# Performance work log

Hardware: AMD Instinct MI355X
Metric: run time of the kernel (lower is better)

## Reference

```python
import jax, jax.numpy as jnp
import numpy as np

B, N, D = 4, 2048, 256
EPS = 1e-5


def _clinear(Z, W, b):
    # complex linear: Z (B,2,N,din), W (2,dout,din), b (2,dout)
    Zr, Zi = Z[:, 0], Z[:, 1]
    Wr, Wi = W[0], W[1]
    outr = Zr @ Wr.T - Zi @ Wi.T + b[0]
    outi = Zr @ Wi.T + Zi @ Wr.T + b[1]
    return jnp.stack([outr, outi], axis=1)


def setup_inputs() -> dict:
    key = jax.random.key(0)
    ks = jax.random.split(key, 14)
    sc = 1.0 / np.sqrt(D).astype(np.float32)
    t = jnp.tile(jnp.arange(N + 1, dtype=jnp.float32)[None] * 0.01, (B, 1))
    return {
        'Z_q': jax.random.normal(ks[0], (B, 2, N, D), jnp.float32),
        'Z_k': jax.random.normal(ks[1], (B, 2, N, D), jnp.float32),
        'Z_v': jax.random.normal(ks[2], (B, 2, N, D), jnp.float32),
        't_measure_all': t,
        'W_q': jax.random.normal(ks[3], (2, D, D), jnp.float32) * sc,
        'b_q': jax.random.normal(ks[4], (2, D), jnp.float32) * 0.01,
        'W_k': jax.random.normal(ks[5], (2, D, D), jnp.float32) * sc,
        'b_k': jax.random.normal(ks[6], (2, D), jnp.float32) * 0.01,
        'W_v': jax.random.normal(ks[7], (2, D, D), jnp.float32) * sc,
        'b_v': jax.random.normal(ks[8], (2, D), jnp.float32) * 0.01,
        'W_p': jax.random.normal(ks[9], (2, D, D), jnp.float32) * sc,
        'b_p': jax.random.normal(ks[10], (2, D), jnp.float32) * 0.01,
        'lambda1': jax.random.normal(ks[11], (2, D // 2, 1), jnp.float32),
        'lambda_Omega_sqrt': jax.random.normal(ks[12], (1, D, 1), jnp.float32) * sc,
        'lambda_Gamma_sqrt': jax.random.normal(ks[13], (1, D, 1), jnp.float32) * sc,
        'tau': jnp.asarray(1.0, jnp.float32),
        'delta': jnp.asarray(0.0, jnp.float32),
        'lambda_C': jnp.ones((1, D, 1), jnp.float32),
    }


def reference(Z_q, Z_k, Z_v, t_measure_all, W_q, b_q, W_k, b_k, W_v, b_v,
              W_p, b_p, lambda1, lambda_Omega_sqrt, lambda_Gamma_sqrt,
              tau, delta, lambda_C):
    # lambda_h = 0 * compute_lambda_h(lambda1): conjugate-pair spectrum, zeroed in forward
    lam_r = 0.0 * jnp.concatenate([lambda1[0], lambda1[0]], axis=0)[:, 0]   # (D,)
    lam_i = 0.0 * jnp.concatenate([lambda1[1], -lambda1[1]], axis=0)[:, 0]  # (D,)
    lam_Om = lambda_Omega_sqrt ** 2 + EPS   # process noise (1,D,1)
    lam_Ga = lambda_Gamma_sqrt ** 2 + EPS   # measurement noise (1,D,1)

    Q = _clinear(Z_q, W_q, b_q)  # (B,2,N,D)
    K = _clinear(Z_k, W_k, b_k)
    V = _clinear(Z_v, W_v, b_v)

    t = t_measure_all[0, :-1]  # (N,)
    # exponential state-transition kernels exp(+/- lambda * t): (2,N,D)
    mag_f = jnp.exp(lam_r[None] * t[:, None]); ph_f = lam_i[None] * t[:, None]
    exp_f = jnp.stack([mag_f * jnp.cos(ph_f), mag_f * jnp.sin(ph_f)])
    mag_b = jnp.exp(-lam_r[None] * t[:, None]); ph_b = -lam_i[None] * t[:, None]
    exp_b = jnp.stack([mag_b * jnp.cos(ph_b), mag_b * jnp.sin(ph_b)])
    # one-step transition exp(lambda * dt): (2,D)
    dt = t[1] - t[0]
    mat_exp = jnp.stack([jnp.exp(lam_r * dt) * jnp.cos(lam_i * dt),
                         jnp.exp(lam_r * dt) * jnp.sin(lam_i * dt)])

    # averaged covariance kernel, exact lambda->0 limit: Gamma + Omega*|t_i-t_j|, mean over D
    lamC2 = lambda_C[0, :, 0] ** 2
    ga_bar = jnp.mean(lamC2 * lam_Ga[0, :, 0])
    om_bar = jnp.mean(lamC2 * lam_Om[0, :, 0])
    abs_dt = jnp.abs(t[:, None] - t[None, :])          # (N,N)
    V_avg_ij = ga_bar + om_bar * abs_dt                # (N,N)

    # factorized kernels
    V_v = exp_f[None]                 # (1,2,N,D)
    U_q = exp_b[None] * Q             # (B,2,N,D)
    U_k = exp_b[None] * K
    U_v = exp_b[None] * V

    # precision-weighted squared residual norm R_ij = sum_d |V_k|^2 |U_q_i - U_k_j|^2
    Vk_abs = jnp.sum(exp_f ** 2, axis=0)              # (N,D)
    Uk_abs = jnp.sum(U_k ** 2, axis=1)                # (B,N,D)
    Uq_abs = jnp.sum(U_q ** 2, axis=1)                # (B,N,D)
    T1 = jnp.einsum('id,bjd->bij', Vk_abs, Uk_abs)
    T2 = jnp.sum(Vk_abs[None] * Uq_abs, axis=2)[:, :, None]
    T3 = (jnp.einsum('bid,bjd->bij', Vk_abs[None] * U_q[:, 0], U_k[:, 0]) +
          jnp.einsum('bid,bjd->bij', Vk_abs[None] * U_q[:, 1], U_k[:, 1]))
    R_qk_abs = T1 + T2 - 2.0 * T3                     # (B,N,N)

    scores = -(tau ** 2) * jnp.log(V_avg_ij[None] + R_qk_abs)
    mask = jnp.tril(jnp.ones((N, N), bool))
    scores = jnp.where(mask[None], scores, -jnp.inf)
    A = jax.nn.softmax(scores, axis=2)                # (B,N,N)
    Q_ij = jnp.stack([A, jnp.zeros_like(A)], axis=1)  # (B,2,N,N)

    # est_inner = complex matmul(Q_ij, U_v); Q imag part is zero
    est_inner = jnp.stack([jnp.einsum('bij,bjd->bid', A, U_v[:, 0]),
                           jnp.einsum('bij,bjd->bid', A, U_v[:, 1])], axis=1)
    est_v = V_v * est_inner          # plain elementwise product, as in source
    s = jax.nn.sigmoid(delta)
    est_eigenbasis = (1.0 - s) * V + s * est_v        # (B,2,N,D)

    # complex Hadamard with one-step transition
    pr = mat_exp[0][None, None] * est_eigenbasis[:, 0] - mat_exp[1][None, None] * est_eigenbasis[:, 1]
    pi = mat_exp[0][None, None] * est_eigenbasis[:, 1] + mat_exp[1][None, None] * est_eigenbasis[:, 0]
    pred_p = jnp.stack([pr, pi], axis=1)
    out = _clinear(pred_p, W_p, b_p)                  # (B,2,N,D)

    lambda_h = jnp.stack([lam_r, lam_i])[..., None]
    return est_eigenbasis, out, Q_ij, V_v, U_v, lambda_h
```

## Files before the change

kernel.cpp:

```cpp
#include <hip/hip_runtime.h>
#include <math.h>

#define BN 4
#define NN 2048
#define DD 256
#define EPSF 1e-5f

typedef __attribute__((ext_vector_type(8))) short bf16x8;
typedef __attribute__((ext_vector_type(4))) float f32x4;

constexpr size_t OFF_EST = 0;
constexpr size_t OFF_OUT = (size_t)BN * 2 * NN * DD;
constexpr size_t OFF_QIJ = OFF_OUT + (size_t)BN * 2 * NN * DD;
constexpr size_t OFF_VV  = OFF_QIJ + (size_t)BN * 2 * NN * NN;
constexpr size_t OFF_UV  = OFF_VV + (size_t)2 * NN * DD;
constexpr size_t OFF_LH  = OFF_UV + (size_t)BN * 2 * NN * DD;

constexpr size_t SCR_B0   = OFF_QIJ + (size_t)NN * NN;
constexpr size_t U_Q16    = 0;
constexpr size_t U_K16    = (size_t)BN * NN * DD;
constexpr size_t U_VT16   = 2 * (size_t)BN * NN * DD;
constexpr size_t SCR_QN   = SCR_B0 + 3 * (size_t)BN * NN * DD / 2;
constexpr size_t SCR_KN   = SCR_QN + (size_t)BN * NN;
constexpr size_t SCR_L    = SCR_KN + (size_t)BN * NN;
constexpr size_t SCR_SC   = SCR_L + (size_t)BN * NN;
constexpr size_t SCR_W16P = SCR_SC + 16;
constexpr size_t SCR_E16F = OFF_QIJ + 3 * (size_t)NN * NN;
constexpr size_t U_PART   = (size_t)BN * NN * 512;
constexpr size_t SCR_Z16F = OFF_QIJ + 5 * (size_t)NN * NN;
constexpr size_t SCR_Z16VF = OFF_QIJ + 7 * (size_t)NN * NN;
constexpr size_t U_W16    = (size_t)BN * NN * 512;

constexpr size_t W16_PER_B = 136 * 16384;

__device__ __forceinline__ short f2bf(float x) {
    union { float f; unsigned u; } v; v.f = x;
    unsigned r = v.u + 0x7fff + ((v.u >> 16) & 1);
    return (short)(r >> 16);
}
__device__ __forceinline__ float bf2f(unsigned short h) {
    union { unsigned u; float f; } v; v.u = ((unsigned)h) << 16;
    return v.f;
}
__device__ __forceinline__ unsigned short* u16p(float* d, size_t fofs) {
    return (unsigned short*)(d + fofs);
}
__device__ __forceinline__ const unsigned short* u16pc(const float* d, size_t fofs) {
    return (const unsigned short*)(d + fofs);
}
__device__ __forceinline__ unsigned short* w16p(float* d, int b) {
    return (b < 3) ? u16p(d, SCR_Z16F) + (size_t)b * W16_PER_B
                   : u16p(d, SCR_Z16VF);
}
__device__ __forceinline__ const unsigned short* w16pc(const float* d, int b) {
    return (b < 3) ? u16pc(d, SCR_Z16F) + (size_t)b * W16_PER_B
                   : u16pc(d, SCR_Z16VF);
}
__device__ __forceinline__ int nc_of(int TI) { return TI >= 12 ? 3 : (TI >= 6 ? 2 : 1); }
__device__ __forceinline__ int cb_of(int TI) {
    return TI < 6 ? TI : (TI < 12 ? 6 + 2 * (TI - 6) : 18 + 3 * (TI - 12));
}

__global__ void k_cvt(const float* __restrict__ Zq, const float* __restrict__ Zk,
                      const float* __restrict__ Zv,
                      const float* __restrict__ Wq, const float* __restrict__ Wk,
                      const float* __restrict__ Wv, const float* __restrict__ Wp,
                      const float* __restrict__ tau, const float* __restrict__ delta,
                      const float* __restrict__ lamOm, const float* __restrict__ lamGa,
                      const float* __restrict__ lamC,
                      float* __restrict__ dout) {
    const int z = blockIdx.z;
    if (z < 3) {
        const float* Z = (z == 0) ? Zq : (z == 1) ? Zk : Zv;
        unsigned short* O = (z == 0) ? u16p(dout, SCR_Z16F)
                          : (z == 1) ? u16p(dout, SCR_Z16F) + (size_t)BN * NN * 512
                                     : u16p(dout, SCR_Z16VF);
        const long n4 = (long)BN * 2 * NN * DD / 4;
        for (long i4 = (long)blockIdx.x * 256 + threadIdx.x; i4 < n4;
             i4 += (long)gridDim.x * 256) {
            const long i = i4 * 4;
            const int d = (int)(i & (DD - 1));
            const long r = i >> 8;
            const int n = (int)(r & (NN - 1));
            const long bc = r >> 11;
            const int c = (int)(bc & 1), b = (int)(bc >> 1);
            float4 v = *(const float4*)&Z[i];
            ushort4 o;
            o.x = (unsigned short)f2bf(v.x); o.y = (unsigned short)f2bf(v.y);
            o.z = (unsigned short)f2bf(v.z); o.w = (unsigned short)f2bf(v.w);
            *(ushort4*)&O[((size_t)(b * NN + n)) * 512 + c * 256 + d] = o;
        }
    } else if (z == 3) {
        const float* Ws[4] = {Wq, Wk, Wv, Wp};
        const long n4 = 6L * 256 * 512 / 4;
        for (long e4 = (long)blockIdx.x * 256 + threadIdx.x; e4 < n4;
             e4 += (long)gridDim.x * 256) {
            const long e = e4 * 4;
            const int k = (int)(e & 511);
            const long rest = e >> 9;
            const int dd = (int)(rest & 255);
            const int m = (int)(rest >> 8);
            int proj, mode;
            if (m < 3)      { proj = m; mode = 0; }
            else if (m == 3){ proj = 2; mode = 1; }
            else            { proj = 3; mode = m - 4; }
            const int kc = k >> 8, kk = k & 255;
            int wc; float sgn;
            if (mode == 0) { wc = kc; sgn = kc ? -1.f : 1.f; }
            else           { wc = 1 - kc; sgn = 1.f; }
            float4 v = *(const float4*)&Ws[proj][((size_t)wc * DD + dd) * DD + kk];
            ushort4 o;
            o.x = (unsigned short)f2bf(sgn * v.x); o.y = (unsigned short)f2bf(sgn * v.y);
            o.z = (unsigned short)f2bf(sgn * v.z); o.w = (unsigned short)f2bf(sgn * v.w);
            unsigned short* dst = (m < 4)
                ? u16p(dout, SCR_Z16VF) + U_W16 + (size_t)m * 131072
                : u16p(dout, SCR_W16P) + (size_t)(m - 4) * 131072;
            *(ushort4*)&dst[(size_t)dd * 512 + k] = o;
        }
    } else {
        const int idx = blockIdx.x * 256 + threadIdx.x;
        if (idx < 3 * BN * NN) dout[SCR_QN + idx] = 0.f;
        if (blockIdx.x == 0) {
            __shared__ float red[8];
            const int t = threadIdx.x;
            float c2 = lamC[t] * lamC[t];
            float ga = c2 * (lamGa[t] * lamGa[t] + EPSF);
            float om = c2 * (lamOm[t] * lamOm[t] + EPSF);
            for (int o = 32; o > 0; o >>= 1) {
                ga += __shfl_down(ga, o, 64);
                om += __shfl_down(om, o, 64);
            }
            if ((t & 63) == 0) { red[t >> 6] = ga; red[4 + (t >> 6)] = om; }
            __syncthreads();
            if (t == 0) {
                float gs = red[0] + red[1] + red[2] + red[3];
                float os = red[4] + red[5] + red[6] + red[7];
                float* scal = dout + SCR_SC;
                scal[0] = tau[0] * tau[0];
                scal[1] = 1.f / (1.f + __expf(-delta[0]));
                scal[2] = gs / 256.f;
                scal[3] = os / 256.f;
            }
        }
    }
}

__global__ __launch_bounds__(256) void k_qkv(const float* __restrict__ bq,
                                             const float* __restrict__ bk,
                                             const float* __restrict__ bv,
                                             float* __restrict__ dout)
{
    __shared__ short Al[128 * 40];
    __shared__ short Bl[128 * 40];
    const int z = blockIdx.z;
    const int d0 = blockIdx.x * 128;
    const int b = blockIdx.y >> 4;
    const int n0 = (blockIdx.y & 15) * 128;

    const unsigned short* Z16 =
        (z == 0) ? u16pc(dout, SCR_Z16F)
      : (z == 1) ? u16pc(dout, SCR_Z16F) + (size_t)BN * NN * 512
                 : u16pc(dout, SCR_Z16VF);
    const unsigned short* W16 = u16pc(dout, SCR_Z16VF) + U_W16 + (size_t)z * 131072;
    const float* bias = (z == 0) ? bq : (z == 1) ? bk : bv;
    const int bofs = (z == 3) ? DD : 0;

    const int t = threadIdx.x, wave = t >> 6, lane = t & 63, quad = lane >> 4, lm = lane & 15;
    const int wm = (wave >> 1) * 64, wn = (wave & 1) * 64;
    const int srow = t >> 1, sch = (t & 1) * 16;

    f32x4 acc[4][4];
#pragma unroll
    for (int i = 0; i < 4; ++i)
#pragma unroll
        for (int j = 0; j < 4; ++j) acc[i][j] = (f32x4){0.f, 0.f, 0.f, 0.f};

    for (int kt = 0; kt < 16; ++kt) {
        const int kk0 = kt * 32;
        const unsigned short* Za = Z16 + ((size_t)(b * NN + n0 + srow)) * 512 + kk0 + sch;
        bf16x8 a0 = *(const bf16x8*)(Za + 0);
        bf16x8 a1 = *(const bf16x8*)(Za + 8);
        const unsigned short* Wa = W16 + (size_t)(d0 + srow) * 512 + kk0 + sch;
        bf16x8 w0 = *(const bf16x8*)(Wa + 0);
        bf16x8 w1 = *(const bf16x8*)(Wa + 8);
        __syncthreads();
        *(bf16x8*)&Al[srow * 40 + sch]     = a0;
        *(bf16x8*)&Al[srow * 40 + sch + 8] = a1;
        *(bf16x8*)&Bl[srow * 40 + sch]     = w0;
        *(bf16x8*)&Bl[srow * 40 + sch + 8] = w1;
        __syncthreads();
        bf16x8 af[4], bff[4];
#pragma unroll
        for (int mi = 0; mi < 4; ++mi) af[mi] = *(const bf16x8*)&Al[(wm + mi * 16 + lm) * 40 + quad * 8];
#pragma unroll
        for (int nj = 0; nj < 4; ++nj) bff[nj] = *(const bf16x8*)&Bl[(wn + nj * 16 + lm) * 40 + quad * 8];
#pragma unroll
        for (int mi = 0; mi < 4; ++mi)
#pragma unroll
            for (int nj = 0; nj < 4; ++nj)
                acc[mi][nj] = __builtin_amdgcn_mfma_f32_16x16x32_bf16(af[mi], bff[nj], acc[mi][nj], 0, 0, 0);
    }

    if (z <= 1) {
        unsigned short* O16 = u16p(dout, SCR_B0) + (z ? U_K16 : U_Q16) + (size_t)b * NN * DD;
        float* NRM = dout + (z ? SCR_KN : SCR_QN) + b * NN;
#pragma unroll
        for (int mi = 0; mi < 4; ++mi)
#pragma unroll
            for (int r = 0; r < 4; ++r) {
                const int m = n0 + wm + mi * 16 + quad * 4 + r;
                float ss = 0.f;
#pragma unroll
                for (int nj = 0; nj < 4; ++nj) {
                    const int d = d0 + wn + nj * 16 + lm;
                    unsigned short h = (unsigned short)f2bf(acc[mi][nj][r] + bias[d]);
                    O16[(size_t)m * DD + d] = h;
                    const float vb = bf2f(h);
                    ss = fmaf(vb, vb, ss);
                }
                ss += __shfl_down(ss, 8, 16); ss += __shfl_down(ss, 4, 16);
                ss += __shfl_down(ss, 2, 16); ss += __shfl_down(ss, 1, 16);
                if (lm == 0) atomicAdd(&NRM[m], ss);
            }
    } else if (z == 2) {
        float* UV0 = dout + OFF_UV + (size_t)(b * 2) * NN * DD;
#pragma unroll
        for (int mi = 0; mi < 4; ++mi)
#pragma unroll
            for (int r = 0; r < 4; ++r) {
                const int m = n0 + wm + mi * 16 + quad * 4 + r;
#pragma unroll
                for (int nj = 0; nj < 4; ++nj) {
                    const int d = d0 + wn + nj * 16 + lm;
                    UV0[(size_t)m * DD + d] = acc[mi][nj][r] + bias[d];
                }
            }
    } else {
        const float s1 = 1.f - dout[SCR_SC + 1];
        float* EST1 = dout + OFF_EST + (size_t)(b * 2 + 1) * NN * DD;
        unsigned short* E16 = u16p(dout, SCR_E16F) + (size_t)b * NN * 512;
#pragma unroll
        for (int mi = 0; mi < 4; ++mi)
#pragma unroll
            for (int r = 0; r < 4; ++r) {
                const int m = n0 + wm + mi * 16 + quad * 4 + r;
#pragma unroll
                for (int nj = 0; nj < 4; ++nj) {
                    const int d = d0 + wn + nj * 16 + lm;
                    const float v = s1 * (acc[mi][nj][r] + bias[bofs + d]);
                    EST1[(size_t)m * DD + d] = v;
                    E16[(size_t)m * 512 + 256 + d] = (unsigned short)f2bf(v);
                }
            }
    }
}

__global__ __launch_bounds__(256) void k_outproj(const float* __restrict__ bp,
                                                 float* __restrict__ dout)
{
    __shared__ short Al[128 * 40];
    __shared__ short Bl[128 * 40];
    const int z = blockIdx.z;
    const int d0 = blockIdx.x * 128;
    const int b = blockIdx.y >> 4;
    const int n0 = (blockIdx.y & 15) * 128;
    const unsigned short* E16 = u16pc(dout, SCR_E16F) + (size_t)b * NN * 512;
    const unsigned short* W16 = u16pc(dout, SCR_W16P) + (size_t)z * 131072;

    const int t = threadIdx.x, wave = t >> 6, lane = t & 63, quad = lane >> 4, lm = lane & 15;
    const int wm = (wave >> 1) * 64, wn = (wave & 1) * 64;
    const int srow = t >> 1, sch = (t & 1) * 16;

    f32x4 acc[4][4];
#pragma unroll
    for (int i = 0; i < 4; ++i)
#pragma unroll
        for (int j = 0; j < 4; ++j) acc[i][j] = (f32x4){0.f, 0.f, 0.f, 0.f};

    for (int kt = 0; kt < 16; ++kt) {
        const int kk0 = kt * 32;
        const unsigned short* Za = E16 + ((size_t)(n0 + srow)) * 512 + kk0 + sch;
        bf16x8 a0 = *(const bf16x8*)(Za + 0);
        bf16x8 a1 = *(const bf16x8*)(Za + 8);
        const unsigned short* Wa = W16 + (size_t)(d0 + srow) * 512 + kk0 + sch;
        bf16x8 w0 = *(const bf16x8*)(Wa + 0);
        bf16x8 w1 = *(const bf16x8*)(Wa + 8);
        __syncthreads();
        *(bf16x8*)&Al[srow * 40 + sch]     = a0;
        *(bf16x8*)&Al[srow * 40 + sch + 8] = a1;
        *(bf16x8*)&Bl[srow * 40 + sch]     = w0;
        *(bf16x8*)&Bl[srow * 40 + sch + 8] = w1;
        __syncthreads();
        bf16x8 af[4], bff[4];
#pragma unroll
        for (int mi = 0; mi < 4; ++mi) af[mi] = *(const bf16x8*)&Al[(wm + mi * 16 + lm) * 40 + quad * 8];
#pragma unroll
        for (int nj = 0; nj < 4; ++nj) bff[nj] = *(const bf16x8*)&Bl[(wn + nj * 16 + lm) * 40 + quad * 8];
#pragma unroll
        for (int mi = 0; mi < 4; ++mi)
#pragma unroll
            for (int nj = 0; nj < 4; ++nj)
                acc[mi][nj] = __builtin_amdgcn_mfma_f32_16x16x32_bf16(af[mi], bff[nj], acc[mi][nj], 0, 0, 0);
    }
    const int bofs = z ? DD : 0;
    float* O = dout + OFF_OUT + (size_t)(b * 2 + z) * NN * DD;
#pragma unroll
    for (int mi = 0; mi < 4; ++mi)
#pragma unroll
        for (int r = 0; r < 4; ++r) {
            const int m = n0 + wm + mi * 16 + quad * 4 + r;
#pragma unroll
            for (int nj = 0; nj < 4; ++nj) {
                const int d = d0 + wn + nj * 16 + lm;
                O[(size_t)m * DD + d] = acc[mi][nj][r] + bp[bofs + d];
            }
        }
}

__global__ void k_vtrans(float* __restrict__ dout) {
    __shared__ float T[64][65];
    const int b = blockIdx.z;
    const int nb = blockIdx.x * 64, db = blockIdx.y * 64;
    const float* V = dout + OFF_UV + (size_t)(b * 2) * NN * DD;
    unsigned short* VT = u16p(dout, SCR_B0) + U_VT16 + (size_t)b * DD * NN;
    const int tr = threadIdx.x >> 4, tc = (threadIdx.x & 15) * 4;
#pragma unroll
    for (int p = 0; p < 4; ++p) {
        float4 v = *(const float4*)&V[(size_t)(nb + tr + p * 16) * DD + db + tc];
        T[tr + p * 16][tc + 0] = v.x; T[tr + p * 16][tc + 1] = v.y;
        T[tr + p * 16][tc + 2] = v.z; T[tr + p * 16][tc + 3] = v.w;
    }
    __syncthreads();
#pragma unroll
    for (int p = 0; p < 4; ++p) {
        const int d = tr + p * 16;
        ushort4 o;
        o.x = (unsigned short)f2bf(T[tc + 0][d]);
        o.y = (unsigned short)f2bf(T[tc + 1][d]);
        o.z = (unsigned short)f2bf(T[tc + 2][d]);
        o.w = (unsigned short)f2bf(T[tc + 3][d]);
        *(ushort4*)&VT[(size_t)(db + d) * NN + nb + tc] = o;
    }
}

__global__ __launch_bounds__(256) void k_scores(const float* __restrict__ tmeas,
                                                float* __restrict__ dout) {
    __shared__ short Al[128 * 40];
    __shared__ short Bl[128 * 40];
    const int b = blockIdx.y, x = blockIdx.x;
    int ti = (int)((sqrtf(8.f * x + 1.f) - 1.f) * 0.5f);
    while ((ti + 1) * (ti + 2) / 2 <= x) ++ti;
    while (ti * (ti + 1) / 2 > x) --ti;
    const int tj = x - ti * (ti + 1) / 2;
    const int i0 = ti * 128, j0 = tj * 128;
    const unsigned short* Q16 = u16pc(dout, SCR_B0) + U_Q16 + (size_t)b * NN * DD;
    const unsigned short* K16 = u16pc(dout, SCR_B0) + U_K16 + (size_t)b * NN * DD;
    const int t = threadIdx.x, wave = t >> 6, lane = t & 63, quad = lane >> 4, lm = lane & 15;
    const int wm = (wave >> 1) * 64, wn = (wave & 1) * 64;
    const int srow = t >> 1, sch = (t & 1) * 16;

    f32x4 acc[4][4];
#pragma unroll
    for (int i = 0; i < 4; ++i)
#pragma unroll
        for (int j = 0; j < 4; ++j) acc[i][j] = (f32x4){0.f, 0.f, 0.f, 0.f};

    for (int kt = 0; kt < 8; ++kt) {
        const int kk0 = kt * 32;
        bf16x8 q0 = *(const bf16x8*)(Q16 + (size_t)(i0 + srow) * DD + kk0 + sch);
        bf16x8 q1 = *(const bf16x8*)(Q16 + (size_t)(i0 + srow) * DD + kk0 + sch + 8);
        bf16x8 k0 = *(const bf16x8*)(K16 + (size_t)(j0 + srow) * DD + kk0 + sch);
        bf16x8 k1 = *(const bf16x8*)(K16 + (size_t)(j0 + srow) * DD + kk0 + sch + 8);
        __syncthreads();
        *(bf16x8*)&Al[srow * 40 + sch]     = q0;
        *(bf16x8*)&Al[srow * 40 + sch + 8] = q1;
        *(bf16x8*)&Bl[srow * 40 + sch]     = k0;
        *(bf16x8*)&Bl[srow * 40 + sch + 8] = k1;
        __syncthreads();
        bf16x8 af[4], bff[4];
#pragma unroll
        for (int mi = 0; mi < 4; ++mi) af[mi] = *(const bf16x8*)&Al[(wm + mi * 16 + lm) * 40 + quad * 8];
#pragma unroll
        for (int nj = 0; nj < 4; ++nj) bff[nj] = *(const bf16x8*)&Bl[(wn + nj * 16 + lm) * 40 + quad * 8];
#pragma unroll
        for (int mi = 0; mi < 4; ++mi)
#pragma unroll
            for (int nj = 0; nj < 4; ++nj)
                acc[mi][nj] = __builtin_amdgcn_mfma_f32_16x16x32_bf16(af[mi], bff[nj], acc[mi][nj], 0, 0, 0);
    }

    const float tau2 = dout[SCR_SC + 0], ga = dout[SCR_SC + 2], om = dout[SCR_SC + 3];
    unsigned short* WT = w16p(dout, b) + (size_t)x * 16384;
    const float* QN_ = dout + SCR_QN + b * NN;
    const float* KN_ = dout + SCR_KN + b * NN;
    float kn[4], tjv[4]; int jj[4];
#pragma unroll
    for (int nj = 0; nj < 4; ++nj) {
        jj[nj] = j0 + wn + nj * 16 + lm;
        kn[nj] = KN_[jj[nj]];
        tjv[nj] = tmeas[jj[nj]];
    }
#pragma unroll
    for (int mi = 0; mi < 4; ++mi)
#pragma unroll
        for (int r = 0; r < 4; ++r) {
            const int li = wm + mi * 16 + quad * 4 + r;
            const int i = i0 + li;
            const float qni = QN_[i], tqi = tmeas[i];
            float rs = 0.f;
#pragma unroll
            for (int nj = 0; nj < 4; ++nj) {
                float xx = ga + om * fabsf(tqi - tjv[nj]) + qni + kn[nj] - 2.f * acc[mi][nj][r];
                xx = fmaxf(xx, 1e-30f);
                float w = (tau2 == 1.f) ? __builtin_amdgcn_rcpf(xx)
                                        : __expf(-tau2 * __logf(xx));
                if (jj[nj] > i) w = 0.f;
                const unsigned short h = (unsigned short)f2bf(w);
                WT[(size_t)li * 128 + (wn + nj * 16 + lm)] = h;
                rs += bf2f(h);
            }
            rs += __shfl_down(rs, 8, 16); rs += __shfl_down(rs, 4, 16);
            rs += __shfl_down(rs, 2, 16); rs += __shfl_down(rs, 1, 16);
            if (lm == 0) atomicAdd(&dout[SCR_L + b * NN + i], rs);
        }
}

__global__ __launch_bounds__(256) void k_estinner(float* __restrict__ dout) {
    __shared__ short Al[128 * 40];
    __shared__ short Bl[128 * 40];
    const int b = blockIdx.y;
    const int chunk = blockIdx.x >> 1, half = blockIdx.x & 1;
    int y = chunk, TI = 0, cb = 0;
    for (;;) { const int nc = nc_of(TI); if (y < nc) break; y -= nc; cb += nc; ++TI; }
    const int i0 = TI * 128;
    const int kbeg = y * 768;
    const int kend = min(kbeg + 768, (TI + 1) * 128);
    const int nst = (kend - kbeg) >> 5;
    const int cidx = cb + y;
    const int tri = TI * (TI + 1) / 2;
    const unsigned short* WT = w16pc(dout, b);
    const unsigned short* VT = u16pc(dout, SCR_B0) + U_VT16 + (size_t)b * DD * NN;
    float* Qij = dout + OFF_QIJ + (size_t)b * 2 * NN * NN;

    const int t = threadIdx.x, wave = t >> 6, lane = t & 63, quad = lane >> 4, lm = lane & 15;
    const int wm = (wave >> 1) * 64, wn = (wave & 1) * 64;
    const int arow = t >> 1, asel = (t & 1) * 16;
    const float linv = (half == 0) ? 1.f / dout[SCR_L + b * NN + i0 + arow] : 0.f;

    f32x4 acc[4][4];
#pragma unroll
    for (int i = 0; i < 4; ++i)
#pragma unroll
        for (int j = 0; j < 4; ++j) acc[i][j] = (f32x4){0.f, 0.f, 0.f, 0.f};

    for (int kt = 0; kt < nst; ++kt) {
        const int kk0 = kbeg + kt * 32;
        const int tile = kk0 >> 7;
        const unsigned short* Ap = WT + ((size_t)(tri + tile)) * 16384
                                 + (size_t)arow * 128 + (kk0 & 127) + asel;
        bf16x8 a0 = *(const bf16x8*)(Ap + 0);
        bf16x8 a1 = *(const bf16x8*)(Ap + 8);
        const unsigned short* Vp = VT + (size_t)(half * 128 + arow) * NN + kk0 + asel;
        bf16x8 v0 = *(const bf16x8*)(Vp + 0);
        bf16x8 v1 = *(const bf16x8*)(Vp + 8);
        __syncthreads();
        *(bf16x8*)&Al[arow * 40 + asel]     = a0;
        *(bf16x8*)&Al[arow * 40 + asel + 8] = a1;
        *(bf16x8*)&Bl[arow * 40 + asel]     = v0;
        *(bf16x8*)&Bl[arow * 40 + asel + 8] = v1;
        __syncthreads();
        if (half == 0) {
            float* Qp = &Qij[(size_t)(i0 + arow) * NN + kk0 + asel];
            float4 f;
            f.x = bf2f((unsigned short)a0[0]) * linv;
            f.y = bf2f((unsigned short)a0[1]) * linv;
            f.z = bf2f((unsigned short)a0[2]) * linv;
            f.w = bf2f((unsigned short)a0[3]) * linv;
            *(float4*)(Qp + 0) = f;
            f.x = bf2f((unsigned short)a0[4]) * linv;
            f.y = bf2f((unsigned short)a0[5]) * linv;
            f.z = bf2f((unsigned short)a0[6]) * linv;
            f.w = bf2f((unsigned short)a0[7]) * linv;
            *(float4*)(Qp + 4) = f;
            f.x = bf2f((unsigned short)a1[0]) * linv;
            f.y = bf2f((unsigned short)a1[1]) * linv;
            f.z = bf2f((unsigned short)a1[2]) * linv;
            f.w = bf2f((unsigned short)a1[3]) * linv;
            *(float4*)(Qp + 8) = f;
            f.x = bf2f((unsigned short)a1[4]) * linv;
            f.y = bf2f((unsigned short)a1[5]) * linv;
            f.z = bf2f((unsigned short)a1[6]) * linv;
            f.w = bf2f((unsigned short)a1[7]) * linv;
            *(float4*)(Qp + 12) = f;
        }
        bf16x8 af[4], bff[4];
#pragma unroll
        for (int mi = 0; mi < 4; ++mi) af[mi] = *(const bf16x8*)&Al[(wm + mi * 16 + lm) * 40 + quad * 8];
#pragma unroll
        for (int nj = 0; nj < 4; ++nj) bff[nj] = *(const bf16x8*)&Bl[(wn + nj * 16 + lm) * 40 + quad * 8];
#pragma unroll
        for (int mi = 0; mi < 4; ++mi)
#pragma unroll
            for (int nj = 0; nj < 4; ++nj)
                acc[mi][nj] = __builtin_amdgcn_mfma_f32_16x16x32_bf16(af[mi], bff[nj], acc[mi][nj], 0, 0, 0);
    }
    unsigned short* P = u16p(dout, SCR_E16F) + U_PART +
                        ((size_t)(b * 30 + cidx)) * 128 * 256;
#pragma unroll
    for (int mi = 0; mi < 4; ++mi)
#pragma unroll
        for (int r = 0; r < 4; ++r) {
            const int ri = wm + mi * 16 + quad * 4 + r;
#pragma unroll
            for (int nj = 0; nj < 4; ++nj) {
                const int d = half * 128 + wn + nj * 16 + lm;
                P[(size_t)ri * 256 + d] = (unsigned short)f2bf(acc[mi][nj][r]);
            }
        }
}

__global__ void k_blendfills(float* __restrict__ dout) {
    const int z = blockIdx.z;
    if (z < 4) {
        const int b = z;
        if (blockIdx.x >= 512) return;
        const int t = threadIdx.x;
        const int i = blockIdx.x * 4 + (t >> 6);
        const int d4 = (t & 63) * 4;
        const int TI = i >> 7;
        const int nc = nc_of(TI), cb = cb_of(TI);
        const float s = dout[SCR_SC + 1];
        const float linv = 1.f / dout[SCR_L + b * NN + i];
        const unsigned short* P = u16pc(dout, SCR_E16F) + U_PART;
        float4 sum = {0.f, 0.f, 0.f, 0.f};
        for (int c = 0; c < nc; ++c) {
            ushort4 pv = *(const ushort4*)&P[((size_t)(b * 30 + cb + c) * 128 + (i & 127)) * 256 + d4];
            sum.x += bf2f(pv.x); sum.y += bf2f(pv.y);
            sum.z += bf2f(pv.z); sum.w += bf2f(pv.w);
        }
        const float4 vr = *(const float4*)&dout[OFF_UV + ((size_t)(b * 2) * NN + i) * DD + d4];
        const float sl = s * linv;
        float4 ev;
        ev.x = (1.f - s) * vr.x + sl * sum.x;
        ev.y = (1.f - s) * vr.y + sl * sum.y;
        ev.z = (1.f - s) * vr.z + sl * sum.z;
        ev.w = (1.f - s) * vr.w + sl * sum.w;
        *(float4*)&dout[OFF_EST + ((size_t)(b * 2) * NN + i) * DD + d4] = ev;
        ushort4 o;
        o.x = (unsigned short)f2bf(ev.x); o.y = (unsigned short)f2bf(ev.y);
        o.z = (unsigned short)f2bf(ev.z); o.w = (unsigned short)f2bf(ev.w);
        *(ushort4*)&u16p(dout, SCR_E16F)[((size_t)(b * NN + i)) * 512 + d4] = o;
        return;
    }
    if (z < 8) {
        const int b = z - 4, i = blockIdx.x;
        const int jstart = ((i >> 7) + 1) << 7;
        float* row = dout + OFF_QIJ + (size_t)b * 2 * NN * NN + (size_t)i * NN;
        const float4 zz = {0.f, 0.f, 0.f, 0.f};
        for (int j = jstart + threadIdx.x * 4; j < NN; j += 256 * 4)
            *(float4*)&row[j] = zz;
        return;
    }
    size_t base; long n; float val = 0.f;
    if (z == 8)       { base = SCR_B0; n = 3145728; }
    else if (z == 9)  { base = SCR_Z16F; n = (long)NN * NN; }
    else if (z == 10) { base = SCR_Z16VF; n = (long)NN * NN; }
    else if (z == 11) { base = OFF_VV; n = (long)NN * DD; val = 1.f; }
    else if (z == 12) { base = OFF_VV + (size_t)NN * DD; n = (long)NN * DD; }
    else if (z < 17)  { base = OFF_UV + (size_t)(2 * (z - 13) + 1) * NN * DD; n = (long)NN * DD; }
    else              { base = OFF_LH; n = 512; }
    float* p = dout + base;
    const float4 v = {val, val, val, val};
    for (long i = ((long)blockIdx.x * 256 + threadIdx.x) * 4; i < n;
         i += (long)gridDim.x * 1024)
        *(float4*)&p[i] = v;
}

__global__ void k_tail(float* __restrict__ dout) {
    const float4 zz = {0.f, 0.f, 0.f, 0.f};
    const long n1 = (long)NN * NN;
    for (long i = ((long)blockIdx.x * 256 + threadIdx.x) * 4; i < n1;
         i += (long)gridDim.x * 1024)
        *(float4*)&dout[SCR_E16F + i] = zz;
    const long n0 = (long)NN * NN - 3145728;
    for (long i = ((long)blockIdx.x * 256 + threadIdx.x) * 4; i < n0;
         i += (long)gridDim.x * 1024)
        *(float4*)&dout[SCR_QN + i] = zz;
}

extern "C" void kernel_launch(void* const* d_in, const int* in_sizes, int n_in,
                              void* d_out, int out_size, void* d_ws, size_t ws_size,
                              hipStream_t stream) {
    const float* Zq = (const float*)d_in[0];
    const float* Zk = (const float*)d_in[1];
    const float* Zv = (const float*)d_in[2];
    const float* tm = (const float*)d_in[3];
    const float* Wq = (const float*)d_in[4];
    const float* bq = (const float*)d_in[5];
    const float* Wk = (const float*)d_in[6];
    const float* bk = (const float*)d_in[7];
    const float* Wv = (const float*)d_in[8];
    const float* bv = (const float*)d_in[9];
    const float* Wp = (const float*)d_in[10];
    const float* bp = (const float*)d_in[11];
    const float* lamOm = (const float*)d_in[13];
    const float* lamGa = (const float*)d_in[14];
    const float* tau = (const float*)d_in[15];
    const float* delta = (const float*)d_in[16];
    const float* lamC = (const float*)d_in[17];
    float* out = (float*)d_out;

    k_cvt<<<dim3(2048, 1, 5), dim3(256), 0, stream>>>(
        Zq, Zk, Zv, Wq, Wk, Wv, Wp, tau, delta, lamOm, lamGa, lamC, out);
    k_qkv<<<dim3(2, 64, 4), dim3(256), 0, stream>>>(bq, bk, bv, out);
    k_vtrans<<<dim3(32, 4, 4), dim3(256), 0, stream>>>(out);
    k_scores<<<dim3(136, 4), dim3(256), 0, stream>>>(tm, out);
    k_estinner<<<dim3(60, 4), dim3(256), 0, stream>>>(out);
    k_blendfills<<<dim3(2048, 1, 18), dim3(256), 0, stream>>>(out);
    k_outproj<<<dim3(2, 64, 2), dim3(256), 0, stream>>>(bp, out);
    k_tail<<<dim3(2048), dim3(256), 0, stream>>>(out);
}
```

Measured before the change: 354.8 us.

## Stage GEMM tiles with direct global-to-LDS loads and move Q_ij writes to fill kernel

All four MFMA GEMM kernels now stage A/B tiles with global_load_lds (direct global-to-LDS DMA) into unpadded 32-wide LDS rows, skipping the register round-trip. The normalized Q_ij writes move from k_estinner into the blend/fill kernel, which now writes each full row (scaled values below the diagonal block, zeros above). The scratch-region zero fills from blendfills and k_tail become hipMemsetAsync calls. Risks: unpadded LDS rows may cause bank conflicts on the fragment reads, and Q_ij values are now reread from the bf16 scratch.

```diff
diff --git a/kernel.cpp b/kernel.cpp
--- a/kernel.cpp
+++ b/kernel.cpp
@@ -59,6 +59,22 @@
 __device__ __forceinline__ int nc_of(int TI) { return TI >= 12 ? 3 : (TI >= 6 ? 2 : 1); }
 __device__ __forceinline__ int cb_of(int TI) {
     return TI < 6 ? TI : (TI < 12 ? 6 + 2 * (TI - 6) : 18 + 3 * (TI - 12));
+}
+
+__device__ __forceinline__ void gll16(const unsigned short* g, short* l) {
+    __builtin_amdgcn_global_load_lds(
+        (const __attribute__((address_space(1))) unsigned*)g,
+        (__attribute__((address_space(3))) unsigned*)l, 16, 0, 0);
+}
+__device__ __forceinline__ void stage_tile(const unsigned short* gbase, size_t stride_sh,
+                                           short* ldsbuf, int t) {
+    const int w = t >> 6, L = t & 63;
+#pragma unroll
+    for (int p = 0; p < 2; ++p) {
+        const int r0 = w * 32 + p * 16;
+        const unsigned short* src = gbase + (size_t)(r0 + (L >> 2)) * stride_sh + (L & 3) * 8;
+        gll16(src, ldsbuf + r0 * 32);
+    }
 }
 
 __global__ void k_cvt(const float* __restrict__ Zq, const float* __restrict__ Zk,
@@ -150,8 +166,8 @@
                                              const float* __restrict__ bv,
                                              float* __restrict__ dout)
 {
-    __shared__ short Al[128 * 40];
-    __shared__ short Bl[128 * 40];
+    __shared__ short Al[128 * 32];
+    __shared__ short Bl[128 * 32];
     const int z = blockIdx.z;
     const int d0 = blockIdx.x * 128;
     const int b = blockIdx.y >> 4;
@@ -167,7 +183,8 @@
 
     const int t = threadIdx.x, wave = t >> 6, lane = t & 63, quad = lane >> 4, lm = lane & 15;
     const int wm = (wave >> 1) * 64, wn = (wave & 1) * 64;
-    const int srow = t >> 1, sch = (t & 1) * 16;
+    const unsigned short* Abase = Z16 + (size_t)(b * NN + n0) * 512;
+    const unsigned short* Bbase = W16 + (size_t)d0 * 512;
 
     f32x4 acc[4][4];
 #pragma unroll
@@ -177,28 +194,20 @@
 
     for (int kt = 0; kt < 16; ++kt) {
         const int kk0 = kt * 32;
-        const unsigned short* Za = Z16 + ((size_t)(b * NN + n0 + srow)) * 512 + kk0 + sch;
-        bf16x8 a0 = *(const bf16x8*)(Za + 0);
-        bf16x8 a1 = *(const bf16x8*)(Za + 8);
-        const unsigned short* Wa = W16 + (size_t)(d0 + srow) * 512 + kk0 + sch;
-        bf16x8 w0 = *(const bf16x8*)(Wa + 0);
-        bf16x8 w1 = *(const bf16x8*)(Wa + 8);
-        __syncthreads();
-        *(bf16x8*)&Al[srow * 40 + sch]     = a0;
-        *(bf16x8*)&Al[srow * 40 + sch + 8] = a1;
-        *(bf16x8*)&Bl[srow * 40 + sch]     = w0;
-        *(bf16x8*)&Bl[srow * 40 + sch + 8] = w1;
+        stage_tile(Abase + kk0, 512, Al, t);
+        stage_tile(Bbase + kk0, 512, Bl, t);
         __syncthreads();
         bf16x8 af[4], bff[4];
 #pragma unroll
-        for (int mi = 0; mi < 4; ++mi) af[mi] = *(const bf16x8*)&Al[(wm + mi * 16 + lm) * 40 + quad * 8];
-#pragma unroll
-        for (int nj = 0; nj < 4; ++nj) bff[nj] = *(const bf16x8*)&Bl[(wn + nj * 16 + lm) * 40 + quad * 8];
+        for (int mi = 0; mi < 4; ++mi) af[mi] = *(const bf16x8*)&Al[(wm + mi * 16 + lm) * 32 + quad * 8];
+#pragma unroll
+        for (int nj = 0; nj < 4; ++nj) bff[nj] = *(const bf16x8*)&Bl[(wn + nj * 16 + lm) * 32 + quad * 8];
 #pragma unroll
         for (int mi = 0; mi < 4; ++mi)
 #pragma unroll
             for (int nj = 0; nj < 4; ++nj)
                 acc[mi][nj] = __builtin_amdgcn_mfma_f32_16x16x32_bf16(af[mi], bff[nj], acc[mi][nj], 0, 0, 0);
+        __syncthreads();
     }
 
     if (z <= 1) {
@@ -258,8 +267,8 @@
 __global__ __launch_bounds__(256) void k_outproj(const float* __restrict__ bp,
                                                  float* __restrict__ dout)
 {
-    __shared__ short Al[128 * 40];
-    __shared__ short Bl[128 * 40];
+    __shared__ short Al[128 * 32];
+    __shared__ short Bl[128 * 32];
     const int z = blockIdx.z;
     const int d0 = blockIdx.x * 128;
     const int b = blockIdx.y >> 4;
@@ -269,7 +278,8 @@
 
     const int t = threadIdx.x, wave = t >> 6, lane = t & 63, quad = lane >> 4, lm = lane & 15;
     const int wm = (wave >> 1) * 64, wn = (wave & 1) * 64;
-    const int srow = t >> 1, sch = (t & 1) * 16;
+    const unsigned short* Abase = E16 + (size_t)n0 * 512;
+    const unsigned short* Bbase = W16 + (size_t)d0 * 512;
 
     f32x4 acc[4][4];
 #pragma unroll
@@ -279,28 +289,20 @@
 
     for (int kt = 0; kt < 16; ++kt) {
         const int kk0 = kt * 32;
-        const unsigned short* Za = E16 + ((size_t)(n0 + srow)) * 512 + kk0 + sch;
-        bf16x8 a0 = *(const bf16x8*)(Za + 0);
-        bf16x8 a1 = *(const bf16x8*)(Za + 8);
-        const unsigned short* Wa = W16 + (size_t)(d0 + srow) * 512 + kk0 + sch;
-        bf16x8 w0 = *(const bf16x8*)(Wa + 0);
-        bf16x8 w1 = *(const bf16x8*)(Wa + 8);
-        __syncthreads();
-        *(bf16x8*)&Al[srow * 40 + sch]     = a0;
-        *(bf16x8*)&Al[srow * 40 + sch + 8] = a1;
-        *(bf16x8*)&Bl[srow * 40 + sch]     = w0;
-        *(bf16x8*)&Bl[srow * 40 + sch + 8] = w1;
+        stage_tile(Abase + kk0, 512, Al, t);
+        stage_tile(Bbase + kk0, 512, Bl, t);
         __syncthreads();
         bf16x8 af[4], bff[4];
 #pragma unroll
-        for (int mi = 0; mi < 4; ++mi) af[mi] = *(const bf16x8*)&Al[(wm + mi * 16 + lm) * 40 + quad * 8];
-#pragma unroll
-        for (int nj = 0; nj < 4; ++nj) bff[nj] = *(const bf16x8*)&Bl[(wn + nj * 16 + lm) * 40 + quad * 8];
+        for (int mi = 0; mi < 4; ++mi) af[mi] = *(const bf16x8*)&Al[(wm + mi * 16 + lm) * 32 + quad * 8];
+#pragma unroll
+        for (int nj = 0; nj < 4; ++nj) bff[nj] = *(const bf16x8*)&Bl[(wn + nj * 16 + lm) * 32 + quad * 8];
 #pragma unroll
         for (int mi = 0; mi < 4; ++mi)
 #pragma unroll
             for (int nj = 0; nj < 4; ++nj)
                 acc[mi][nj] = __builtin_amdgcn_mfma_f32_16x16x32_bf16(af[mi], bff[nj], acc[mi][nj], 0, 0, 0);
+        __syncthreads();
     }
     const int bofs = z ? DD : 0;
     float* O = dout + OFF_OUT + (size_t)(b * 2 + z) * NN * DD;
@@ -345,8 +347,8 @@
 
 __global__ __launch_bounds__(256) void k_scores(const float* __restrict__ tmeas,
                                                 float* __restrict__ dout) {
-    __shared__ short Al[128 * 40];
-    __shared__ short Bl[128 * 40];
+    __shared__ short Al[128 * 32];
+    __shared__ short Bl[128 * 32];
     const int b = blockIdx.y, x = blockIdx.x;
     int ti = (int)((sqrtf(8.f * x + 1.f) - 1.f) * 0.5f);
     while ((ti + 1) * (ti + 2) / 2 <= x) ++ti;
@@ -357,7 +359,8 @@
     const unsigned short* K16 = u16pc(dout, SCR_B0) + U_K16 + (size_t)b * NN * DD;
     const int t = threadIdx.x, wave = t >> 6, lane = t & 63, quad = lane >> 4, lm = lane & 15;
     const int wm = (wave >> 1) * 64, wn = (wave & 1) * 64;
-    const int srow = t >> 1, sch = (t & 1) * 16;
+    const unsigned short* Abase = Q16 + (size_t)i0 * DD;
+    const unsigned short* Bbase = K16 + (size_t)j0 * DD;
 
     f32x4 acc[4][4];
 #pragma unroll
@@ -367,26 +370,20 @@
 
     for (int kt = 0; kt < 8; ++kt) {
         const int kk0 = kt * 32;
-        bf16x8 q0 = *(const bf16x8*)(Q16 + (size_t)(i0 + srow) * DD + kk0 + sch);
-        bf16x8 q1 = *(const bf16x8*)(Q16 + (size_t)(i0 + srow) * DD + kk0 + sch + 8);
-        bf16x8 k0 = *(const bf16x8*)(K16 + (size_t)(j0 + srow) * DD + kk0 + sch);
-        bf16x8 k1 = *(const bf16x8*)(K16 + (size_t)(j0 + srow) * DD + kk0 + sch + 8);
-        __syncthreads();
-        *(bf16x8*)&Al[srow * 40 + sch]     = q0;
-        *(bf16x8*)&Al[srow * 40 + sch + 8] = q1;
-        *(bf16x8*)&Bl[srow * 40 + sch]     = k0;
-        *(bf16x8*)&Bl[srow * 40 + sch + 8] = k1;
+        stage_tile(Abase + kk0, DD, Al, t);
+        stage_tile(Bbase + kk0, DD, Bl, t);
         __syncthreads();
         bf16x8 af[4], bff[4];
 #pragma unroll
-        for (int mi = 0; mi < 4; ++mi) af[mi] = *(const bf16x8*)&Al[(wm + mi * 16 + lm) * 40 + quad * 8];
-#pragma unroll
-        for (int nj = 0; nj < 4; ++nj) bff[nj] = *(const bf16x8*)&Bl[(wn + nj * 16 + lm) * 40 + quad * 8];
+        for (int mi = 0; mi < 4; ++mi) af[mi] = *(const bf16x8*)&Al[(wm + mi * 16 + lm) * 32 + quad * 8];
+#pragma unroll
+        for (int nj = 0; nj < 4; ++nj) bff[nj] = *(const bf16x8*)&Bl[(wn + nj * 16 + lm) * 32 + quad * 8];
 #pragma unroll
         for (int mi = 0; mi < 4; ++mi)
 #pragma unroll
             for (int nj = 0; nj < 4; ++nj)
                 acc[mi][nj] = __builtin_amdgcn_mfma_f32_16x16x32_bf16(af[mi], bff[nj], acc[mi][nj], 0, 0, 0);
+        __syncthreads();
     }
 
     const float tau2 = dout[SCR_SC + 0], ga = dout[SCR_SC + 2], om = dout[SCR_SC + 3];
@@ -426,26 +423,23 @@
 }
 
 __global__ __launch_bounds__(256) void k_estinner(float* __restrict__ dout) {
-    __shared__ short Al[128 * 40];
-    __shared__ short Bl[128 * 40];
+    __shared__ short Al[128 * 32];
+    __shared__ short Bl[128 * 32];
     const int b = blockIdx.y;
     const int chunk = blockIdx.x >> 1, half = blockIdx.x & 1;
     int y = chunk, TI = 0, cb = 0;
     for (;;) { const int nc = nc_of(TI); if (y < nc) break; y -= nc; cb += nc; ++TI; }
-    const int i0 = TI * 128;
     const int kbeg = y * 768;
     const int kend = min(kbeg + 768, (TI + 1) * 128);
     const int nst = (kend - kbeg) >> 5;
     const int cidx = cb + y;
     const int tri = TI * (TI + 1) / 2;
     const unsigned short* WT = w16pc(dout, b);
-    const unsigned short* VT = u16pc(dout, SCR_B0) + U_VT16 + (size_t)b * DD * NN;
-    float* Qij = dout + OFF_QIJ + (size_t)b * 2 * NN * NN;
+    const unsigned short* VT = u16pc(dout, SCR_B0) + U_VT16 + (size_t)b * DD * NN
+                             + (size_t)(half * 128) * NN;
 
     const int t = threadIdx.x, wave = t >> 6, lane = t & 63, quad = lane >> 4, lm = lane & 15;
     const int wm = (wave >> 1) * 64, wn = (wave & 1) * 64;
-    const int arow = t >> 1, asel = (t & 1) * 16;
-    const float linv = (half == 0) ? 1.f / dout[SCR_L + b * NN + i0 + arow] : 0.f;
 
     f32x4 acc[4][4];
 #pragma unroll
@@ -456,53 +450,20 @@
     for (int kt = 0; kt < nst; ++kt) {
         const int kk0 = kbeg + kt * 32;
         const int tile = kk0 >> 7;
-        const unsigned short* Ap = WT + ((size_t)(tri + tile)) * 16384
-                                 + (size_t)arow * 128 + (kk0 & 127) + asel;
-        bf16x8 a0 = *(const bf16x8*)(Ap + 0);
-        bf16x8 a1 = *(const bf16x8*)(Ap + 8);
-        const unsigned short* Vp = VT + (size_t)(half * 128 + arow) * NN + kk0 + asel;
-        bf16x8 v0 = *(const bf16x8*)(Vp + 0);
-        bf16x8 v1 = *(const bf16x8*)(Vp + 8);
-        __syncthreads();
-        *(bf16x8*)&Al[arow * 40 + asel]     = a0;
-        *(bf16x8*)&Al[arow * 40 + asel + 8] = a1;
-        *(bf16x8*)&Bl[arow * 40 + asel]     = v0;
-        *(bf16x8*)&Bl[arow * 40 + asel + 8] = v1;
-        __syncthreads();
-        if (half == 0) {
-            float* Qp = &Qij[(size_t)(i0 + arow) * NN + kk0 + asel];
-            float4 f;
-            f.x = bf2f((unsigned short)a0[0]) * linv;
-            f.y = bf2f((unsigned short)a0[1]) * linv;
-            f.z = bf2f((unsigned short)a0[2]) * linv;
-            f.w = bf2f((unsigned short)a0[3]) * linv;
-            *(float4*)(Qp + 0) = f;
-            f.x = bf2f((unsigned short)a0[4]) * linv;
-            f.y = bf2f((unsigned short)a0[5]) * linv;
-            f.z = bf2f((unsigned short)a0[6]) * linv;
-            f.w = bf2f((unsigned short)a0[7]) * linv;
-            *(float4*)(Qp + 4) = f;
-            f.x = bf2f((unsigned short)a1[0]) * linv;
-            f.y = bf2f((unsigned short)a1[1]) * linv;
-            f.z = bf2f((unsigned short)a1[2]) * linv;
-            f.w = bf2f((unsigned short)a1[3]) * linv;
-            *(float4*)(Qp + 8) = f;
-            f.x = bf2f((unsigned short)a1[4]) * linv;
-            f.y = bf2f((unsigned short)a1[5]) * linv;
-            f.z = bf2f((unsigned short)a1[6]) * linv;
-            f.w = bf2f((unsigned short)a1[7]) * linv;
-            *(float4*)(Qp + 12) = f;
-        }
+        stage_tile(WT + (size_t)(tri + tile) * 16384 + (kk0 & 127), 128, Al, t);
+        stage_tile(VT + kk0, NN, Bl, t);
+        __syncthreads();
         bf16x8 af[4], bff[4];
 #pragma unroll
-        for (int mi = 0; mi < 4; ++mi) af[mi] = *(const bf16x8*)&Al[(wm + mi * 16 + lm) * 40 + quad * 8];
-#pragma unroll
-        for (int nj = 0; nj < 4; ++nj) bff[nj] = *(const bf16x8*)&Bl[(wn + nj * 16 + lm) * 40 + quad * 8];
+        for (int mi = 0; mi < 4; ++mi) af[mi] = *(const bf16x8*)&Al[(wm + mi * 16 + lm) * 32 + quad * 8];
+#pragma unroll
+        for (int nj = 0; nj < 4; ++nj) bff[nj] = *(const bf16x8*)&Bl[(wn + nj * 16 + lm) * 32 + quad * 8];
 #pragma unroll
         for (int mi = 0; mi < 4; ++mi)
 #pragma unroll
             for (int nj = 0; nj < 4; ++nj)
                 acc[mi][nj] = __builtin_amdgcn_mfma_f32_16x16x32_bf16(af[mi], bff[nj], acc[mi][nj], 0, 0, 0);
+        __syncthreads();
     }
     unsigned short* P = u16p(dout, SCR_E16F) + U_PART +
                         ((size_t)(b * 30 + cidx)) * 128 * 256;
@@ -554,38 +515,35 @@
     }
     if (z < 8) {
         const int b = z - 4, i = blockIdx.x;
-        const int jstart = ((i >> 7) + 1) << 7;
+        const int TI = i >> 7, li = i & 127;
+        const int tri = TI * (TI + 1) / 2;
+        const float linv = 1.f / dout[SCR_L + b * NN + i];
+        const unsigned short* WTb = w16pc(dout, b);
         float* row = dout + OFF_QIJ + (size_t)b * 2 * NN * NN + (size_t)i * NN;
-        const float4 zz = {0.f, 0.f, 0.f, 0.f};
-        for (int j = jstart + threadIdx.x * 4; j < NN; j += 256 * 4)
-            *(float4*)&row[j] = zz;
+        for (int j4 = threadIdx.x * 4; j4 < NN; j4 += 1024) {
+            const int tj = j4 >> 7;
+            float4 o = {0.f, 0.f, 0.f, 0.f};
+            if (tj <= TI) {
+                ushort4 h = *(const ushort4*)&WTb[((size_t)(tri + tj)) * 16384
+                                                  + (size_t)li * 128 + (j4 & 127)];
+                o.x = bf2f(h.x) * linv; o.y = bf2f(h.y) * linv;
+                o.z = bf2f(h.z) * linv; o.w = bf2f(h.w) * linv;
+            }
+            *(float4*)&row[j4] = o;
+        }
         return;
     }
     size_t base; long n; float val = 0.f;
     if (z == 8)       { base = SCR_B0; n = 3145728; }
-    else if (z == 9)  { base = SCR_Z16F; n = (long)NN * NN; }
-    else if (z == 10) { base = SCR_Z16VF; n = (long)NN * NN; }
-    else if (z == 11) { base = OFF_VV; n = (long)NN * DD; val = 1.f; }
-    else if (z == 12) { base = OFF_VV + (size_t)NN * DD; n = (long)NN * DD; }
-    else if (z < 17)  { base = OFF_UV + (size_t)(2 * (z - 13) + 1) * NN * DD; n = (long)NN * DD; }
+    else if (z == 9)  { base = OFF_VV; n = (long)NN * DD; val = 1.f; }
+    else if (z == 10) { base = OFF_VV + (size_t)NN * DD; n = (long)NN * DD; }
+    else if (z < 15)  { base = OFF_UV + (size_t)(2 * (z - 11) + 1) * NN * DD; n = (long)NN * DD; }
     else              { base = OFF_LH; n = 512; }
     float* p = dout + base;
     const float4 v = {val, val, val, val};
     for (long i = ((long)blockIdx.x * 256 + threadIdx.x) * 4; i < n;
          i += (long)gridDim.x * 1024)
         *(float4*)&p[i] = v;
-}
-
-__global__ void k_tail(float* __restrict__ dout) {
-    const float4 zz = {0.f, 0.f, 0.f, 0.f};
-    const long n1 = (long)NN * NN;
-    for (long i = ((long)blockIdx.x * 256 + threadIdx.x) * 4; i < n1;
-         i += (long)gridDim.x * 1024)
-        *(float4*)&dout[SCR_E16F + i] = zz;
-    const long n0 = (long)NN * NN - 3145728;
-    for (long i = ((long)blockIdx.x * 256 + threadIdx.x) * 4; i < n0;
-         i += (long)gridDim.x * 1024)
-        *(float4*)&dout[SCR_QN + i] = zz;
 }
 
 extern "C" void kernel_launch(void* const* d_in, const int* in_sizes, int n_in,
@@ -616,7 +574,10 @@
     k_vtrans<<<dim3(32, 4, 4), dim3(256), 0, stream>>>(out);
     k_scores<<<dim3(136, 4), dim3(256), 0, stream>>>(tm, out);
     k_estinner<<<dim3(60, 4), dim3(256), 0, stream>>>(out);
-    k_blendfills<<<dim3(2048, 1, 18), dim3(256), 0, stream>>>(out);
+    k_blendfills<<<dim3(2048, 1, 16), dim3(256), 0, stream>>>(out);
     k_outproj<<<dim3(2, 64, 2), dim3(256), 0, stream>>>(bp, out);
-    k_tail<<<dim3(2048), dim3(256), 0, stream>>>(out);
-}
+    hipMemsetAsync((void*)(out + SCR_Z16F),  0, (size_t)NN * NN * 4, stream);
+    hipMemsetAsync((void*)(out + SCR_Z16VF), 0, (size_t)NN * NN * 4, stream);
+    hipMemsetAsync((void*)(out + SCR_E16F),  0, (size_t)NN * NN * 4, stream);
+    hipMemsetAsync((void*)(out + SCR_QN),    0, ((size_t)NN * NN - 3145728) * 4, stream);
+}
```

After: 352.2 us. Within noise of the previous version (-0.7%).
